# Kernel tuning notes

Hardware: AMD Instinct MI355X
Metric: run time of the kernel (lower is better)

Reference implementation:

```python
import jax, jax.numpy as jnp
import numpy as np

N_NODES = 50000
N_EDGES = 1200000
IN_CH = 128
HID = 64
HEADS = 1
OUT_CH = 64
NEG_SLOPE = 0.2


def setup_inputs() -> dict:
    key = jax.random.key(0)
    ks = jax.random.split(key, 9)
    x = jax.random.normal(ks[0], (N_NODES, IN_CH), dtype=jnp.float32)
    edge_index = jax.random.randint(ks[1], (2, N_EDGES), 0, N_NODES, dtype=jnp.int64)
    edge_weight = jax.random.uniform(ks[2], (N_EDGES,), dtype=jnp.float32)
    # GATv2Conv params: separate lin_l / lin_r (share_weights=False), attention vector, bias
    s_in = 1.0 / np.sqrt(IN_CH)
    W_l = jax.random.uniform(ks[3], (HEADS * HID, IN_CH), minval=-s_in, maxval=s_in, dtype=jnp.float32)
    W_r = jax.random.uniform(ks[4], (HEADS * HID, IN_CH), minval=-s_in, maxval=s_in, dtype=jnp.float32)
    att = jax.random.normal(ks[5], (HEADS, HID), dtype=jnp.float32) * (1.0 / np.sqrt(HID))
    bias_conv = jnp.zeros((HEADS * HID,), dtype=jnp.float32)
    s_h = 1.0 / np.sqrt(HEADS * HID)
    W_lin = jax.random.uniform(ks[6], (OUT_CH, HEADS * HID), minval=-s_h, maxval=s_h, dtype=jnp.float32)
    b_lin = jax.random.uniform(ks[7], (OUT_CH,), minval=-s_h, maxval=s_h, dtype=jnp.float32)
    return {"x": x, "edge_index": edge_index, "edge_weight": edge_weight,
            "W_l": W_l, "W_r": W_r, "att": att, "bias_conv": bias_conv,
            "W_lin": W_lin, "b_lin": b_lin}


def reference(x, edge_index, edge_weight, W_l, W_r, att, bias_conv, W_lin, b_lin):
    N = x.shape[0]
    H, C = att.shape
    # add self loops (GATv2Conv default add_self_loops=True)
    loop = jnp.arange(N, dtype=edge_index.dtype)
    src = jnp.concatenate([edge_index[0], loop])  # [E+N] source j
    dst = jnp.concatenate([edge_index[1], loop])  # [E+N] target i
    # linear projections -> [N, H, C]
    xl = (x @ W_l.T).reshape(N, H, C)
    xr = (x @ W_r.T).reshape(N, H, C)
    # per-edge GATv2 logits: att . LeakyReLU(xl_j + xr_i)
    e = jax.nn.leaky_relu(xl[src] + xr[dst], NEG_SLOPE)       # [E, H, C]
    logits = jnp.einsum('ehc,hc->eh', e, att)                 # [E, H]
    # segment softmax over incoming edges of each target node
    m = jax.ops.segment_max(logits, dst, num_segments=N)       # [N, H]
    m = jnp.where(jnp.isfinite(m), m, 0.0)
    expv = jnp.exp(logits - m[dst])                            # [E, H]
    denom = jax.ops.segment_sum(expv, dst, num_segments=N)     # [N, H]
    alpha = expv / (denom[dst] + 1e-16)                        # [E, H]
    # dropout(p=0.2) on alpha: identity in eval mode
    # scatter-weighted aggregation of source features
    msg = alpha[:, :, None] * xl[src]                          # [E, H, C]
    out = jax.ops.segment_sum(msg, dst, num_segments=N)        # [N, H, C]
    out = out.reshape(N, H * C) + bias_conv
    out = jax.nn.elu(out)
    return out @ W_lin.T + b_lin
```

## Files before the change

kernel.cpp:

```cpp
#include <hip/hip_runtime.h>

#define IN_CH 128
#define HID 64
#define NEG 0.2f

typedef short bf16x8 __attribute__((ext_vector_type(8)));
typedef float f32x4  __attribute__((ext_vector_type(4)));

__device__ __forceinline__ unsigned short f2bf(float f) {
    unsigned u = __float_as_uint(f);
    u += 0x7fffu + ((u >> 16) & 1u);
    return (unsigned short)(u >> 16);
}
__device__ __forceinline__ float bf2f(unsigned short h) {
    return __uint_as_float((unsigned)h << 16);
}

__global__ __launch_bounds__(512, 4) void proj_part(
    const float* __restrict__ x, const float* __restrict__ W_l,
    const float* __restrict__ W_r,
    unsigned short* __restrict__ xlb, float* __restrict__ xr,
    const int* __restrict__ src, const int* __restrict__ dst,
    int* __restrict__ gcursor, unsigned* __restrict__ pairs,
    int nN, int E)
{
    __shared__ unsigned short A_hi[64 * 136];
    __shared__ unsigned short A_lo[64 * 136];
    int tid = threadIdx.x;
    int nb = blockIdx.x * 64;
    int lane = tid & 63;
    int wid = __builtin_amdgcn_readfirstlane(tid >> 6);
    int mat = wid >> 2;
    int ct  = (wid & 3) * 16;
    int n = lane & 15, quad = lane >> 4;

    const float* __restrict__ W = mat ? W_r : W_l;
    bf16x8 Bh[4], Bl[4];
    #pragma unroll
    for (int s = 0; s < 4; ++s) {
        const float* wr = W + (size_t)(ct + n) * IN_CH + s * 32 + quad * 8;
        float4 w0 = *(const float4*)(wr);
        float4 w1 = *(const float4*)(wr + 4);
        float wf[8] = {w0.x, w0.y, w0.z, w0.w, w1.x, w1.y, w1.z, w1.w};
        #pragma unroll
        for (int j = 0; j < 8; ++j) {
            unsigned short h = f2bf(wf[j]);
            Bh[s][j] = (short)h;
            Bl[s][j] = (short)f2bf(wf[j] - bf2f(h));
        }
    }

    #pragma unroll
    for (int it = 0; it < 2; ++it) {
        int gi = it * 512 + tid;
        int row = gi >> 4, c8 = gi & 15;
        int node = nb + row;
        uint4 hi = make_uint4(0, 0, 0, 0), lo = make_uint4(0, 0, 0, 0);
        if (node < nN) {
            const float* xp = x + (size_t)node * IN_CH + c8 * 8;
            float4 f0 = *(const float4*)(xp);
            float4 f1 = *(const float4*)(xp + 4);
            float xf[8] = {f0.x, f0.y, f0.z, f0.w, f1.x, f1.y, f1.z, f1.w};
            unsigned hh[8], ll[8];
            #pragma unroll
            for (int j = 0; j < 8; ++j) {
                unsigned short h = f2bf(xf[j]);
                hh[j] = h;
                ll[j] = f2bf(xf[j] - bf2f(h));
            }
            hi = make_uint4(hh[0] | (hh[1] << 16), hh[2] | (hh[3] << 16),
                            hh[4] | (hh[5] << 16), hh[6] | (hh[7] << 16));
            lo = make_uint4(ll[0] | (ll[1] << 16), ll[2] | (ll[3] << 16),
                            ll[4] | (ll[5] << 16), ll[6] | (ll[7] << 16));
        }
        *(uint4*)(&A_hi[row * 136 + c8 * 8]) = hi;
        *(uint4*)(&A_lo[row * 136 + c8 * 8]) = lo;
    }
    __syncthreads();

    #pragma unroll
    for (int mt = 0; mt < 4; ++mt) {
        f32x4 d = {0.f, 0.f, 0.f, 0.f};
        int arow = (mt * 16 + n) * 136 + quad * 8;
        #pragma unroll
        for (int s = 0; s < 4; ++s) {
            bf16x8 ah = *(const bf16x8*)(&A_hi[arow + s * 32]);
            bf16x8 al = *(const bf16x8*)(&A_lo[arow + s * 32]);
            d = __builtin_amdgcn_mfma_f32_16x16x32_bf16(ah, Bh[s], d, 0, 0, 0);
            d = __builtin_amdgcn_mfma_f32_16x16x32_bf16(ah, Bl[s], d, 0, 0, 0);
            d = __builtin_amdgcn_mfma_f32_16x16x32_bf16(al, Bh[s], d, 0, 0, 0);
        }
        #pragma unroll
        for (int r = 0; r < 4; ++r) {
            int node = nb + mt * 16 + quad * 4 + r;
            if (node < nN) {
                if (mat)
                    xr[(size_t)node * HID + ct + n] = d[r];
                else
                    xlb[(size_t)node * HID + ct + n] = f2bf(d[r]);
            }
        }
    }

    __syncthreads();
    int* lh = (int*)A_hi;
    int* lb = lh + 1024;
    for (int i = tid; i < 1024; i += 512) lh[i] = 0;
    __syncthreads();

    int G = (int)gridDim.x;
    int C = ((E + G - 1) / G + 3) & ~3;
    int lo = blockIdx.x * C;
    int hi = lo + C; if (hi > E) hi = E;

    int i0 = lo + tid * 4;
    unsigned pay[4];
    int bk[4], rk[4];
    int ne = 0;
    if (i0 + 3 < hi) {
        int4 s4 = *(const int4*)(src + i0);
        int4 d4 = *(const int4*)(dst + i0);
        bk[0] = d4.x >> 6; pay[0] = (unsigned)s4.x | (((unsigned)d4.x & 63u) << 16);
        bk[1] = d4.y >> 6; pay[1] = (unsigned)s4.y | (((unsigned)d4.y & 63u) << 16);
        bk[2] = d4.z >> 6; pay[2] = (unsigned)s4.z | (((unsigned)d4.z & 63u) << 16);
        bk[3] = d4.w >> 6; pay[3] = (unsigned)s4.w | (((unsigned)d4.w & 63u) << 16);
        ne = 4;
        #pragma unroll
        for (int q = 0; q < 4; ++q) rk[q] = atomicAdd(&lh[bk[q]], 1);
    } else {
        for (int j = i0; j < hi; ++j) {
            int s = src[j], d = dst[j];
            bk[ne] = d >> 6;
            pay[ne] = (unsigned)s | (((unsigned)d & 63u) << 16);
            rk[ne] = atomicAdd(&lh[bk[ne]], 1);
            ++ne;
        }
    }
    __syncthreads();
    for (int i = tid; i < 1024; i += 512) {
        int c = lh[i];
        lb[i] = c ? atomicAdd(&gcursor[i], c) : 0;
    }
    __syncthreads();
    for (int q = 0; q < ne; ++q) {
        int p = lb[bk[q]] + rk[q];
        if (p < 2048) pairs[(bk[q] << 11) + p] = pay[q];
    }
}

__global__ __launch_bounds__(256, 8) void gat_sorted(
    const unsigned short* __restrict__ xlb, const float* __restrict__ xr,
    const unsigned* __restrict__ pairs, const int* __restrict__ bcnt,
    const float* __restrict__ att, const float* __restrict__ bias_conv,
    const float* __restrict__ W_lin, const float* __restrict__ b_lin,
    float* __restrict__ out, int nN)
{
    __shared__ unsigned short sorted[2048];
    __shared__ unsigned short Hhi[32 * 72];
    __shared__ unsigned short Hlo[32 * 72];
    __shared__ int cnt[32];
    __shared__ int rs[33];
    __shared__ int cur[32];
    int tid = threadIdx.x;
    if (tid < 32) cnt[tid] = 0;
    __syncthreads();

    int blk = blockIdx.x;
    int b  = blk >> 1;
    int hh = blk & 1;
    int M = bcnt[b];
    if (M > 2048) M = 2048;
    const unsigned* __restrict__ pb = pairs + ((size_t)b << 11);

    unsigned ew[8];
    int ne = 0;
    for (int i = tid; i < M; i += 256) {
        unsigned w = pb[i];
        int d6 = (w >> 16) & 63;
        if ((d6 >> 5) == hh) {
            ew[ne++] = w;
            atomicAdd(&cnt[d6 & 31], 1);
        }
    }
    __syncthreads();
    if (tid < 32) {
        int c = cnt[tid];
        int s = c;
        #pragma unroll
        for (int d = 1; d < 32; d <<= 1) {
            int t = __shfl_up(s, d, 64);
            if (tid >= d) s += t;
        }
        rs[tid] = s - c;
        cur[tid] = s - c;
        if (tid == 31) rs[32] = s;
    }
    __syncthreads();
    for (int q = 0; q < ne; ++q) {
        unsigned w = ew[q];
        int d = (w >> 16) & 31;
        int p = atomicAdd(&cur[d], 1);
        sorted[p] = (unsigned short)(w & 0xFFFFu);
    }
    __syncthreads();

    int lane = tid & 63, wv = tid >> 6;
    int g = lane >> 4, gl = lane & 15;
    const float4 att4 = *(const float4*)(att + gl * 4);
    const float c1 = 0.5f * (1.f + NEG), c2 = 0.5f * (1.f - NEG);
    float4 a1 = make_float4(c1 * att4.x, c1 * att4.y, c1 * att4.z, c1 * att4.w);
    float4 a2 = make_float4(c2 * att4.x, c2 * att4.y, c2 * att4.z, c2 * att4.w);
    int nb = b * 64 + hh * 32;
    for (int t = 0; t < 8; ++t) {
        int nl = wv * 8 + t;
        int node = nb + nl;
        if (node >= nN) break;
        const float4 xr4 = *(const float4*)(xr + (size_t)node * HID + gl * 4);
        float4 acc = make_float4(0.f, 0.f, 0.f, 0.f);
        float denom = 0.f;
        if (g == 0) {
            ushort4 us = *(const ushort4*)(xlb + (size_t)node * HID + gl * 4);
            float xsx = bf2f(us.x), xsy = bf2f(us.y), xsz = bf2f(us.z), xsw = bf2f(us.w);
            float tx = xsx + xr4.x, ty = xsy + xr4.y;
            float tz = xsz + xr4.z, tw = xsw + xr4.w;
            float r = a1.x * tx;
            r = fmaf(a2.x, fabsf(tx), r);
            r = fmaf(a1.y, ty, r); r = fmaf(a2.y, fabsf(ty), r);
            r = fmaf(a1.z, tz, r); r = fmaf(a2.z, fabsf(tz), r);
            r = fmaf(a1.w, tw, r); r = fmaf(a2.w, fabsf(tw), r);
            r += __shfl_xor(r, 1, 64);
            r += __shfl_xor(r, 2, 64);
            r += __shfl_xor(r, 4, 64);
            r += __shfl_xor(r, 8, 64);
            float ev = __expf(r);
            denom = ev;
            acc.x = ev * xsx; acc.y = ev * xsy;
            acc.z = ev * xsz; acc.w = ev * xsw;
        }
        int s0 = rs[nl], s1 = rs[nl + 1];
        int last = s1 - 1;
        for (int base = s0; base < s1; base += 16) {
            int kb = base + g * 4;
            int k0 = (kb     <= last) ? kb     : last;
            int k1 = (kb + 1 <= last) ? kb + 1 : last;
            int k2 = (kb + 2 <= last) ? kb + 2 : last;
            int k3 = (kb + 3 <= last) ? kb + 3 : last;
            int j0 = sorted[k0], j1 = sorted[k1], j2 = sorted[k2], j3 = sorted[k3];
            ushort4 ua = *(const ushort4*)(xlb + (size_t)j0 * HID + gl * 4);
            ushort4 ub = *(const ushort4*)(xlb + (size_t)j1 * HID + gl * 4);
            ushort4 uc = *(const ushort4*)(xlb + (size_t)j2 * HID + gl * 4);
            ushort4 ud = *(const ushort4*)(xlb + (size_t)j3 * HID + gl * 4);
            float xax = bf2f(ua.x), xay = bf2f(ua.y), xaz = bf2f(ua.z), xaw = bf2f(ua.w);
            float xbx = bf2f(ub.x), xby = bf2f(ub.y), xbz = bf2f(ub.z), xbw = bf2f(ub.w);
            float xcx = bf2f(uc.x), xcy = bf2f(uc.y), xcz = bf2f(uc.z), xcw = bf2f(uc.w);
            float xdx = bf2f(ud.x), xdy = bf2f(ud.y), xdz = bf2f(ud.z), xdw = bf2f(ud.w);

            float t0, t1, t2, t3, ra, rb, rc, rd;
            t0 = xax + xr4.x; t1 = xay + xr4.y; t2 = xaz + xr4.z; t3 = xaw + xr4.w;
            ra = a1.x * t0;        ra = fmaf(a2.x, fabsf(t0), ra);
            ra = fmaf(a1.y, t1, ra); ra = fmaf(a2.y, fabsf(t1), ra);
            ra = fmaf(a1.z, t2, ra); ra = fmaf(a2.z, fabsf(t2), ra);
            ra = fmaf(a1.w, t3, ra); ra = fmaf(a2.w, fabsf(t3), ra);
            t0 = xbx + xr4.x; t1 = xby + xr4.y; t2 = xbz + xr4.z; t3 = xbw + xr4.w;
            rb = a1.x * t0;        rb = fmaf(a2.x, fabsf(t0), rb);
            rb = fmaf(a1.y, t1, rb); rb = fmaf(a2.y, fabsf(t1), rb);
            rb = fmaf(a1.z, t2, rb); rb = fmaf(a2.z, fabsf(t2), rb);
            rb = fmaf(a1.w, t3, rb); rb = fmaf(a2.w, fabsf(t3), rb);
            t0 = xcx + xr4.x; t1 = xcy + xr4.y; t2 = xcz + xr4.z; t3 = xcw + xr4.w;
            rc = a1.x * t0;        rc = fmaf(a2.x, fabsf(t0), rc);
            rc = fmaf(a1.y, t1, rc); rc = fmaf(a2.y, fabsf(t1), rc);
            rc = fmaf(a1.z, t2, rc); rc = fmaf(a2.z, fabsf(t2), rc);
            rc = fmaf(a1.w, t3, rc); rc = fmaf(a2.w, fabsf(t3), rc);
            t0 = xdx + xr4.x; t1 = xdy + xr4.y; t2 = xdz + xr4.z; t3 = xdw + xr4.w;
            rd = a1.x * t0;        rd = fmaf(a2.x, fabsf(t0), rd);
            rd = fmaf(a1.y, t1, rd); rd = fmaf(a2.y, fabsf(t1), rd);
            rd = fmaf(a1.z, t2, rd); rd = fmaf(a2.z, fabsf(t2), rd);
            rd = fmaf(a1.w, t3, rd); rd = fmaf(a2.w, fabsf(t3), rd);

            ra += __shfl_xor(ra, 1, 64); rb += __shfl_xor(rb, 1, 64);
            rc += __shfl_xor(rc, 1, 64); rd += __shfl_xor(rd, 1, 64);
            ra += __shfl_xor(ra, 2, 64); rb += __shfl_xor(rb, 2, 64);
            rc += __shfl_xor(rc, 2, 64); rd += __shfl_xor(rd, 2, 64);
            ra += __shfl_xor(ra, 4, 64); rb += __shfl_xor(rb, 4, 64);
            rc += __shfl_xor(rc, 4, 64); rd += __shfl_xor(rd, 4, 64);
            ra += __shfl_xor(ra, 8, 64); rb += __shfl_xor(rb, 8, 64);
            rc += __shfl_xor(rc, 8, 64); rd += __shfl_xor(rd, 8, 64);

            float ea = (kb     < s1) ? __expf(ra) : 0.f;
            float eb = (kb + 1 < s1) ? __expf(rb) : 0.f;
            float ec = (kb + 2 < s1) ? __expf(rc) : 0.f;
            float ed = (kb + 3 < s1) ? __expf(rd) : 0.f;
            denom += (ea + eb) + (ec + ed);
            acc.x = fmaf(ea, xax, acc.x); acc.x = fmaf(eb, xbx, acc.x);
            acc.x = fmaf(ec, xcx, acc.x); acc.x = fmaf(ed, xdx, acc.x);
            acc.y = fmaf(ea, xay, acc.y); acc.y = fmaf(eb, xby, acc.y);
            acc.y = fmaf(ec, xcy, acc.y); acc.y = fmaf(ed, xdy, acc.y);
            acc.z = fmaf(ea, xaz, acc.z); acc.z = fmaf(eb, xbz, acc.z);
            acc.z = fmaf(ec, xcz, acc.z); acc.z = fmaf(ed, xdz, acc.z);
            acc.w = fmaf(ea, xaw, acc.w); acc.w = fmaf(eb, xbw, acc.w);
            acc.w = fmaf(ec, xcw, acc.w); acc.w = fmaf(ed, xdw, acc.w);
        }
        denom += __shfl_xor(denom, 16, 64);
        denom += __shfl_xor(denom, 32, 64);
        acc.x += __shfl_xor(acc.x, 16, 64); acc.x += __shfl_xor(acc.x, 32, 64);
        acc.y += __shfl_xor(acc.y, 16, 64); acc.y += __shfl_xor(acc.y, 32, 64);
        acc.z += __shfl_xor(acc.z, 16, 64); acc.z += __shfl_xor(acc.z, 32, 64);
        acc.w += __shfl_xor(acc.w, 16, 64); acc.w += __shfl_xor(acc.w, 32, 64);
        float inv = 1.f / (denom + 1e-16f);
        float4 b4 = *(const float4*)(bias_conv + gl * 4);
        float hx = fmaf(acc.x, inv, b4.x);
        float hy = fmaf(acc.y, inv, b4.y);
        float hz = fmaf(acc.z, inv, b4.z);
        float hw = fmaf(acc.w, inv, b4.w);
        hx = (hx > 0.f) ? hx : (__expf(hx) - 1.f);
        hy = (hy > 0.f) ? hy : (__expf(hy) - 1.f);
        hz = (hz > 0.f) ? hz : (__expf(hz) - 1.f);
        hw = (hw > 0.f) ? hw : (__expf(hw) - 1.f);
        if (g == 0) {
            unsigned short hix = f2bf(hx), hiy = f2bf(hy),
                           hiz = f2bf(hz), hiw = f2bf(hw);
            ushort4 vhi = make_ushort4(hix, hiy, hiz, hiw);
            ushort4 vlo = make_ushort4(f2bf(hx - bf2f(hix)), f2bf(hy - bf2f(hiy)),
                                       f2bf(hz - bf2f(hiz)), f2bf(hw - bf2f(hiw)));
            *(ushort4*)(&Hhi[nl * 72 + gl * 4]) = vhi;
            *(ushort4*)(&Hlo[nl * 72 + gl * 4]) = vlo;
        }
    }
    __syncthreads();

    bf16x8 Wh[2], Wl[2];
    #pragma unroll
    for (int s = 0; s < 2; ++s) {
        const float* wr = W_lin + (size_t)(wv * 16 + gl) * HID + s * 32 + g * 8;
        float4 w0 = *(const float4*)(wr);
        float4 w1 = *(const float4*)(wr + 4);
        float wf[8] = {w0.x, w0.y, w0.z, w0.w, w1.x, w1.y, w1.z, w1.w};
        #pragma unroll
        for (int j = 0; j < 8; ++j) {
            unsigned short h = f2bf(wf[j]);
            Wh[s][j] = (short)h;
            Wl[s][j] = (short)f2bf(wf[j] - bf2f(h));
        }
    }
    float blin = b_lin[wv * 16 + gl];
    #pragma unroll
    for (int mt = 0; mt < 2; ++mt) {
        f32x4 d = {0.f, 0.f, 0.f, 0.f};
        int arow = (mt * 16 + gl) * 72 + g * 8;
        #pragma unroll
        for (int s = 0; s < 2; ++s) {
            bf16x8 ah = *(const bf16x8*)(&Hhi[arow + s * 32]);
            bf16x8 al = *(const bf16x8*)(&Hlo[arow + s * 32]);
            d = __builtin_amdgcn_mfma_f32_16x16x32_bf16(ah, Wh[s], d, 0, 0, 0);
            d = __builtin_amdgcn_mfma_f32_16x16x32_bf16(ah, Wl[s], d, 0, 0, 0);
            d = __builtin_amdgcn_mfma_f32_16x16x32_bf16(al, Wh[s], d, 0, 0, 0);
        }
        #pragma unroll
        for (int r = 0; r < 4; ++r) {
            int node = nb + mt * 16 + g * 4 + r;
            if (node < nN)
                out[(size_t)node * HID + wv * 16 + gl] = d[r] + blin;
        }
    }
}

extern "C" void kernel_launch(void* const* d_in, const int* in_sizes, int n_in,
                              void* d_out, int out_size, void* d_ws, size_t ws_size,
                              hipStream_t stream) {
    const float* x      = (const float*)d_in[0];
    const int*   ei     = (const int*)d_in[1];
    const float* W_l    = (const float*)d_in[3];
    const float* W_r    = (const float*)d_in[4];
    const float* att    = (const float*)d_in[5];
    const float* bias_c = (const float*)d_in[6];
    const float* W_lin  = (const float*)d_in[7];
    const float* b_lin  = (const float*)d_in[8];
    float* out = (float*)d_out;

    int N = in_sizes[0] / IN_CH;
    int E = in_sizes[2];
    const int* srcp = ei;
    const int* dstp = ei + E;
    int NB = (N + 63) / 64;

    char* ws = (char*)d_ws;
    float* xr = (float*)ws;
    unsigned short* xlb = (unsigned short*)(xr + (size_t)N * HID);
    int* gcursor = (int*)(xlb + (size_t)N * HID);
    unsigned* pairs = (unsigned*)(gcursor + 1024);

    hipMemsetAsync(gcursor, 0, 1024 * sizeof(int), stream);
    proj_part<<<NB, 512, 0, stream>>>(x, W_l, W_r, xlb, xr, srcp, dstp,
                                      gcursor, pairs, N, E);
    gat_sorted<<<NB * 2, 256, 0, stream>>>(xlb, xr, pairs, gcursor,
                                           att, bias_c, W_lin, b_lin, out, N);
}
```

Baseline: 173.6 us.

## Shrink destination buckets to 16 nodes and sort with precomputed ranks

The edge partition now buckets by 16 destination nodes instead of 64, with 512-slot buckets and a 4096-entry cursor table. The aggregation kernel handles one whole bucket per block, so it no longer scans 64-node buckets and discards half the edges. Its per-destination counting sort also reuses the ranks returned by the first atomic, removing a second atomic pass. The trade-offs are four times more global cursor atomics and histogram work in the partition kernel, a single MFMA tile per block in the output projection, and silent truncation if a 16-node bucket ever receives more than 512 edges.

```diff
diff --git a/kernel.cpp b/kernel.cpp
--- a/kernel.cpp
+++ b/kernel.cpp
@@ -104,8 +104,8 @@
 
     __syncthreads();
     int* lh = (int*)A_hi;
-    int* lb = lh + 1024;
-    for (int i = tid; i < 1024; i += 512) lh[i] = 0;
+    int* lb = (int*)A_lo;
+    for (int i = tid; i < 4096; i += 512) lh[i] = 0;
     __syncthreads();
 
     int G = (int)gridDim.x;
@@ -120,31 +120,31 @@
     if (i0 + 3 < hi) {
         int4 s4 = *(const int4*)(src + i0);
         int4 d4 = *(const int4*)(dst + i0);
-        bk[0] = d4.x >> 6; pay[0] = (unsigned)s4.x | (((unsigned)d4.x & 63u) << 16);
-        bk[1] = d4.y >> 6; pay[1] = (unsigned)s4.y | (((unsigned)d4.y & 63u) << 16);
-        bk[2] = d4.z >> 6; pay[2] = (unsigned)s4.z | (((unsigned)d4.z & 63u) << 16);
-        bk[3] = d4.w >> 6; pay[3] = (unsigned)s4.w | (((unsigned)d4.w & 63u) << 16);
+        bk[0] = d4.x >> 4; pay[0] = (unsigned)s4.x | (((unsigned)d4.x & 15u) << 16);
+        bk[1] = d4.y >> 4; pay[1] = (unsigned)s4.y | (((unsigned)d4.y & 15u) << 16);
+        bk[2] = d4.z >> 4; pay[2] = (unsigned)s4.z | (((unsigned)d4.z & 15u) << 16);
+        bk[3] = d4.w >> 4; pay[3] = (unsigned)s4.w | (((unsigned)d4.w & 15u) << 16);
         ne = 4;
         #pragma unroll
         for (int q = 0; q < 4; ++q) rk[q] = atomicAdd(&lh[bk[q]], 1);
     } else {
         for (int j = i0; j < hi; ++j) {
             int s = src[j], d = dst[j];
-            bk[ne] = d >> 6;
-            pay[ne] = (unsigned)s | (((unsigned)d & 63u) << 16);
+            bk[ne] = d >> 4;
+            pay[ne] = (unsigned)s | (((unsigned)d & 15u) << 16);
             rk[ne] = atomicAdd(&lh[bk[ne]], 1);
             ++ne;
         }
     }
     __syncthreads();
-    for (int i = tid; i < 1024; i += 512) {
+    for (int i = tid; i < 4096; i += 512) {
         int c = lh[i];
         lb[i] = c ? atomicAdd(&gcursor[i], c) : 0;
     }
     __syncthreads();
     for (int q = 0; q < ne; ++q) {
         int p = lb[bk[q]] + rk[q];
-        if (p < 2048) pairs[(bk[q] << 11) + p] = pay[q];
+        if (p < 512) pairs[(bk[q] << 9) + p] = pay[q];
     }
 }
 
@@ -155,53 +155,45 @@
     const float* __restrict__ W_lin, const float* __restrict__ b_lin,
     float* __restrict__ out, int nN)
 {
-    __shared__ unsigned short sorted[2048];
-    __shared__ unsigned short Hhi[32 * 72];
-    __shared__ unsigned short Hlo[32 * 72];
-    __shared__ int cnt[32];
-    __shared__ int rs[33];
-    __shared__ int cur[32];
+    __shared__ unsigned short sorted[512];
+    __shared__ unsigned short Hhi[16 * 72];
+    __shared__ unsigned short Hlo[16 * 72];
+    __shared__ int cnt[16];
+    __shared__ int rs[17];
     int tid = threadIdx.x;
-    if (tid < 32) cnt[tid] = 0;
+    if (tid < 16) cnt[tid] = 0;
     __syncthreads();
 
     int blk = blockIdx.x;
-    int b  = blk >> 1;
-    int hh = blk & 1;
-    int M = bcnt[b];
-    if (M > 2048) M = 2048;
-    const unsigned* __restrict__ pb = pairs + ((size_t)b << 11);
-
-    unsigned ew[8];
+    int M = bcnt[blk];
+    if (M > 512) M = 512;
+    const unsigned* __restrict__ pb = pairs + ((size_t)blk << 9);
+
+    unsigned ew[2];
+    int dl[2], rk[2];
     int ne = 0;
     for (int i = tid; i < M; i += 256) {
         unsigned w = pb[i];
-        int d6 = (w >> 16) & 63;
-        if ((d6 >> 5) == hh) {
-            ew[ne++] = w;
-            atomicAdd(&cnt[d6 & 31], 1);
-        }
-    }
-    __syncthreads();
-    if (tid < 32) {
+        ew[ne] = w;
+        dl[ne] = (w >> 16) & 15;
+        rk[ne] = atomicAdd(&cnt[dl[ne]], 1);
+        ++ne;
+    }
+    __syncthreads();
+    if (tid < 16) {
         int c = cnt[tid];
         int s = c;
         #pragma unroll
-        for (int d = 1; d < 32; d <<= 1) {
+        for (int d = 1; d < 16; d <<= 1) {
             int t = __shfl_up(s, d, 64);
             if (tid >= d) s += t;
         }
         rs[tid] = s - c;
-        cur[tid] = s - c;
-        if (tid == 31) rs[32] = s;
-    }
-    __syncthreads();
-    for (int q = 0; q < ne; ++q) {
-        unsigned w = ew[q];
-        int d = (w >> 16) & 31;
-        int p = atomicAdd(&cur[d], 1);
-        sorted[p] = (unsigned short)(w & 0xFFFFu);
-    }
+        if (tid == 15) rs[16] = s;
+    }
+    __syncthreads();
+    for (int q = 0; q < ne; ++q)
+        sorted[rs[dl[q]] + rk[q]] = (unsigned short)(ew[q] & 0xFFFFu);
     __syncthreads();
 
     int lane = tid & 63, wv = tid >> 6;
@@ -210,9 +202,9 @@
     const float c1 = 0.5f * (1.f + NEG), c2 = 0.5f * (1.f - NEG);
     float4 a1 = make_float4(c1 * att4.x, c1 * att4.y, c1 * att4.z, c1 * att4.w);
     float4 a2 = make_float4(c2 * att4.x, c2 * att4.y, c2 * att4.z, c2 * att4.w);
-    int nb = b * 64 + hh * 32;
-    for (int t = 0; t < 8; ++t) {
-        int nl = wv * 8 + t;
+    int nb = blk * 16;
+    for (int t = 0; t < 4; ++t) {
+        int nl = wv * 4 + t;
         int node = nb + nl;
         if (node >= nN) break;
         const float4 xr4 = *(const float4*)(xr + (size_t)node * HID + gl * 4);
@@ -343,10 +335,9 @@
         }
     }
     float blin = b_lin[wv * 16 + gl];
-    #pragma unroll
-    for (int mt = 0; mt < 2; ++mt) {
+    {
         f32x4 d = {0.f, 0.f, 0.f, 0.f};
-        int arow = (mt * 16 + gl) * 72 + g * 8;
+        int arow = gl * 72 + g * 8;
         #pragma unroll
         for (int s = 0; s < 2; ++s) {
             bf16x8 ah = *(const bf16x8*)(&Hhi[arow + s * 32]);
@@ -357,7 +348,7 @@
         }
         #pragma unroll
         for (int r = 0; r < 4; ++r) {
-            int node = nb + mt * 16 + g * 4 + r;
+            int node = nb + g * 4 + r;
             if (node < nN)
                 out[(size_t)node * HID + wv * 16 + gl] = d[r] + blin;
         }
@@ -382,16 +373,17 @@
     const int* srcp = ei;
     const int* dstp = ei + E;
     int NB = (N + 63) / 64;
+    int NQ = (N + 15) / 16;
 
     char* ws = (char*)d_ws;
     float* xr = (float*)ws;
     unsigned short* xlb = (unsigned short*)(xr + (size_t)N * HID);
     int* gcursor = (int*)(xlb + (size_t)N * HID);
-    unsigned* pairs = (unsigned*)(gcursor + 1024);
-
-    hipMemsetAsync(gcursor, 0, 1024 * sizeof(int), stream);
+    unsigned* pairs = (unsigned*)(gcursor + 4096);
+
+    hipMemsetAsync(gcursor, 0, 4096 * sizeof(int), stream);
     proj_part<<<NB, 512, 0, stream>>>(x, W_l, W_r, xlb, xr, srcp, dstp,
                                       gcursor, pairs, N, E);
-    gat_sorted<<<NB * 2, 256, 0, stream>>>(xlb, xr, pairs, gcursor,
-                                           att, bias_c, W_lin, b_lin, out, N);
-}
+    gat_sorted<<<NQ, 256, 0, stream>>>(xlb, xr, pairs, gcursor,
+                                       att, bias_c, W_lin, b_lin, out, N);
+}
```

New measurement: 176.3 us. About the same (+1.6%).
